# Kernel optimization log

Measured on AMD Instinct MI355X. Metric: run time of the kernel, lower is better.

The kernel has to match this reference:

```python
import jax, jax.numpy as jnp
import numpy as np

N = 100000      # nodes
EG = 600000     # global (knn) edges used by GAT layers
E = 600000      # prediction edges scored by edge_mlp
H = 1           # gat_heads
C = 64          # hidden_dim (per-head out channels)
HC = H * C
EDGE_IN = 2 * HC + 2  # 130
EDGE_HID = EDGE_IN * 4  # 520


def gat_layer(x, W, att_src, att_dst, bias, src, dst):
    # PyG GATConv (concat=True, residual=False, no edge_dim, eval mode)
    n = x.shape[0]
    h = (x @ W).reshape(n, H, C)                      # [N,H,C]
    a_s = jnp.sum(h * att_src, axis=-1)               # [N,H]
    a_d = jnp.sum(h * att_dst, axis=-1)               # [N,H]
    alpha = jax.nn.leaky_relu(a_s[src] + a_d[dst], 0.2)  # [Eg,H]
    amax = jax.ops.segment_max(alpha, dst, num_segments=n)
    amax = jnp.where(jnp.isfinite(amax), amax, 0.0)
    e = jnp.exp(alpha - amax[dst])
    denom = jax.ops.segment_sum(e, dst, num_segments=n)
    w = e / (denom[dst] + 1e-16)                      # scatter-softmax over in-edges of dst
    out = jax.ops.segment_sum(h[src] * w[:, :, None], dst, num_segments=n)
    return out.reshape(n, HC) + bias


def setup_inputs() -> dict:
    key = jax.random.key(0)
    ks = jax.random.split(key, 16)
    glorot = lambda k, shape: jax.random.normal(k, shape, jnp.float32) * np.sqrt(2.0 / (shape[0] + shape[-1]))
    inp = {
        "pos": jax.random.normal(ks[0], (N, 3), jnp.float32),
        "edge_index": jax.random.randint(ks[1], (2, E), 0, N, jnp.int32),
        "global_edge_index": jax.random.randint(ks[2], (2, EG), 0, N, jnp.int32),
        "edge_attr": jax.random.uniform(ks[3], (E, 2), jnp.float32),
        # GAT layer 0 (in=3)
        "W0": glorot(ks[4], (3, HC)),
        "att_src0": glorot(ks[5], (1, H, C)),
        "att_dst0": glorot(ks[6], (1, H, C)),
        "b0": jnp.zeros((HC,), jnp.float32),
        # GAT layer 1 (in=HC)
        "W1": glorot(ks[7], (HC, HC)),
        "att_src1": glorot(ks[8], (1, H, C)),
        "att_dst1": glorot(ks[9], (1, H, C)),
        "b1": jnp.zeros((HC,), jnp.float32),
        # edge MLP: Linear(130,520) -> ELU -> Linear(520,1)
        "Wm1": glorot(ks[10], (EDGE_IN, EDGE_HID)),
        "bm1": jnp.zeros((EDGE_HID,), jnp.float32),
        "Wm2": glorot(ks[11], (EDGE_HID, 1)),
        "bm2": jnp.zeros((1,), jnp.float32),
    }
    return inp


def reference(pos, edge_index, global_edge_index, edge_attr,
              W0, att_src0, att_dst0, b0,
              W1, att_src1, att_dst1, b1,
              Wm1, bm1, Wm2, bm2):
    gsrc, gdst = global_edge_index[0], global_edge_index[1]
    x = pos  # dropout p=0 -> identity
    x = jax.nn.elu(gat_layer(x, W0, att_src0, att_dst0, b0, gsrc, gdst))
    x = jax.nn.elu(gat_layer(x, W1, att_src1, att_dst1, b1, gsrc, gdst))
    # per-edge gather-concat-MLP
    esrc, edst = edge_index[0], edge_index[1]
    ef = jnp.concatenate([x[esrc], x[edst], edge_attr], axis=1)  # [E, 130]
    h = jax.nn.elu(ef @ Wm1 + bm1)
    edge_values = (h @ Wm2 + bm2)[:, 0]  # [E]
    return edge_values
```

## Files before the change

### kernel.cpp

```cpp
#include <hip/hip_runtime.h>

#define KN 100000
#define KEG 600000
#define KE 600000
#define NB 98
#define LOG2E 1.4426950408889634f
#define LN2 0.6931471805599453f

#define FB_PREP 391
#define FB_CVEC 33
#define FB_HIST 2344
#define FB_T0 25000

using u16 = unsigned short;
typedef __bf16 bf16x8 __attribute__((ext_vector_type(8)));
typedef float f32x4 __attribute__((ext_vector_type(4)));
typedef float f32x2 __attribute__((ext_vector_type(2)));

__device__ __forceinline__ float b2f(u16 u) { return __uint_as_float(((unsigned)u) << 16); }
__device__ __forceinline__ u16 f2b(float f) {
  unsigned u = __float_as_uint(f);
  u += 0x7FFF + ((u >> 16) & 1);
  return (u16)(u >> 16);
}
__device__ __forceinline__ int imin(int a, int b) { return a < b ? a : b; }
__device__ __forceinline__ float fexp2(float x) {
#if __has_builtin(__builtin_amdgcn_exp2f)
  return __builtin_amdgcn_exp2f(x);
#else
  return __expf(x * LN2);
#endif
}

__device__ __forceinline__ void gload_lds16(const void* g, void* l) {
  __builtin_amdgcn_global_load_lds(
      (const __attribute__((address_space(1))) unsigned int*)g,
      (__attribute__((address_space(3))) unsigned int*)l,
      16, 0, 0);
}

__global__ __launch_bounds__(256) void k_front(
    const float* __restrict__ pos, const float* __restrict__ W0,
    const float* __restrict__ att_s, const float* __restrict__ att_d,
    const float* __restrict__ wm1, const float* __restrict__ bm1,
    const float* __restrict__ wm2, const float* __restrict__ w1,
    const int* __restrict__ gdst,
    u16* __restrict__ wm1t, u16* __restrict__ w1t, float2* __restrict__ wsc2,
    float* __restrict__ w2sum, int* __restrict__ counts,
    u16* __restrict__ h, float* __restrict__ a_s, float* __restrict__ a_d) {
  int bid = blockIdx.x;
  if (bid < FB_PREP) {
    int idx = bid * 256 + threadIdx.x;
    if (idx < 33 * 5 * 512) {
      int j = idx & 7;
      int lane = (idx >> 3) & 63;
      int f = (idx >> 9) % 5;
      int nt = idx / (512 * 5);
      int n = nt * 16 + (lane & 15);
      float v = 0.f;
      if (n < 520) {
        if (f < 4) {
          int k = f * 32 + (lane >> 4) * 8 + j;
          v = wm1[k * 520 + n] * LOG2E;
        } else {
          int kk = (lane >> 4) * 8 + j;
          if (kk == 0) v = wm1[128 * 520 + n] * LOG2E;
          else if (kk == 1) v = wm1[129 * 520 + n] * LOG2E;
          else if (kk == 2) v = bm1[n] * LOG2E;
        }
      }
      wm1t[idx] = f2b(v);
    }
    if (idx < 33 * 64) {
      int lane = idx & 63, nt = idx >> 6;
      int col = nt * 16 + (lane & 15);
      float w2 = (col < 520) ? wm2[col] : 0.f;
      float2 p; p.x = w2; p.y = -LN2 * w2;
      wsc2[idx] = p;
    }
    if (idx < 4 * 2 * 64 * 8) {
      int j = idx & 7;
      int lane = (idx >> 3) & 63;
      int kt = (idx >> 9) & 1;
      int nt = idx >> 10;
      int n = nt * 16 + (lane & 15);
      int k = kt * 32 + (lane >> 4) * 8 + j;
      w1t[idx] = f2b(w1[k * 64 + n]);
    }
  } else if (bid < FB_PREP + FB_CVEC) {
    int lane = threadIdx.x & 63;
    int w = (bid - FB_PREP) * 4 + (threadIdx.x >> 6);
    float x = 0.f;
    if (w <= 129) {
      const float* row = wm1 + (size_t)w * 520;
#pragma unroll
      for (int j = 0; j < 8; ++j) x += row[j * 64 + lane] * wm2[j * 64 + lane];
      if (lane < 8) x += row[512 + lane] * wm2[512 + lane];
    } else if (w == 130) {
#pragma unroll
      for (int j = 0; j < 8; ++j) x += bm1[j * 64 + lane] * wm2[j * 64 + lane];
      if (lane < 8) x += bm1[512 + lane] * wm2[512 + lane];
    } else if (w == 131) {
#pragma unroll
      for (int j = 0; j < 8; ++j) x += wm2[j * 64 + lane];
      if (lane < 8) x += wm2[512 + lane];
    }
    for (int off = 1; off < 64; off <<= 1) x += __shfl_xor(x, off);
    if (w <= 130 && lane < 16) {
      int f = w >> 5, kk = w & 31;
      int qq = kk >> 3, jj = kk & 7;
      u16 chi = f2b(x);
      float v = (lane == 0) ? x : (lane == 1 ? (x - b2f(chi)) : 0.f);
      wm1t[(33 * 5 + f) * 512 + (qq * 16 + lane) * 8 + jj] = f2b(v);
    } else if (w == 131 && lane == 0) {
      w2sum[0] = x;
    }
  } else if (bid < FB_PREP + FB_CVEC + FB_HIST) {
    int e = (bid - (FB_PREP + FB_CVEC)) * 256 + threadIdx.x;
    if (e < KEG) atomicAdd(counts + gdst[e], 1);
  } else {
    int lane = threadIdx.x & 63;
    int n = (bid - (FB_PREP + FB_CVEC + FB_HIST)) * 4 + (threadIdx.x >> 6);
    float p0 = pos[n * 3 + 0], p1 = pos[n * 3 + 1], p2 = pos[n * 3 + 2];
    float hv = p0 * W0[lane] + p1 * W0[64 + lane] + p2 * W0[128 + lane];
    h[n * 64 + lane] = f2b(hv);
    float s = hv * att_s[lane];
    float d = hv * att_d[lane];
    for (int off = 1; off < 64; off <<= 1) { s += __shfl_xor(s, off); d += __shfl_xor(d, off); }
    if (lane == 0) { a_s[n] = s; a_d[n] = d; }
  }
}


__global__ __launch_bounds__(1024) void k_scan_block(
    const int* __restrict__ counts, int* __restrict__ incl, int* __restrict__ bsum) {
  int gid = blockIdx.x * 1024 + threadIdx.x;
  int lane = threadIdx.x & 63, w = threadIdx.x >> 6;
  int x = (gid < KN) ? counts[gid] : 0;
  for (int off = 1; off < 64; off <<= 1) {
    int y = __shfl_up(x, off);
    if (lane >= off) x += y;
  }
  __shared__ int wtot[16];
  if (lane == 63) wtot[w] = x;
  __syncthreads();
  if (w == 0 && lane < 16) {
    int t = wtot[lane];
    for (int off = 1; off < 16; off <<= 1) {
      int y = __shfl_up(t, off);
      if (lane >= off) t += y;
    }
    wtot[lane] = t;
  }
  __syncthreads();
  if (w > 0) x += wtot[w - 1];
  if (gid < KN) incl[gid] = x;
  if (threadIdx.x == 1023) bsum[blockIdx.x] = x;
}

__global__ __launch_bounds__(64) void k_scan_bsum(const int* __restrict__ bsum, int* __restrict__ boff) {
  int lane = threadIdx.x;
  int x0 = (lane < NB) ? bsum[lane] : 0;
  int x1 = (64 + lane < NB) ? bsum[64 + lane] : 0;
  int i0 = x0, i1 = x1;
  for (int off = 1; off < 64; off <<= 1) {
    int y0 = __shfl_up(i0, off), y1 = __shfl_up(i1, off);
    if (lane >= off) { i0 += y0; i1 += y1; }
  }
  int tot0 = __shfl(i0, 63);
  if (lane < NB) boff[lane] = i0 - x0;
  if (64 + lane < NB) boff[64 + lane] = i1 - x1 + tot0;
}

__global__ __launch_bounds__(1024) void k_scan_final(
    const int* __restrict__ incl, const int* __restrict__ counts,
    const int* __restrict__ boff, int* __restrict__ row_start) {
  int gid = blockIdx.x * 1024 + threadIdx.x;
  if (gid < KN) row_start[gid] = incl[gid] - counts[gid] + boff[blockIdx.x];
}

__global__ __launch_bounds__(256) void k_fill(
    const int* __restrict__ gsrc, const int* __restrict__ gdst,
    const int* __restrict__ row_start, int* __restrict__ cursor,
    int* __restrict__ csr_src) {
  int e = blockIdx.x * 256 + threadIdx.x;
  if (e >= KEG) return;
  int d = gdst[e];
  int pos = atomicAdd(cursor + d, 1);
  csr_src[row_start[d] + pos] = gsrc[e];
}


__global__ __launch_bounds__(256) void k_aggt1(
    const int* __restrict__ row_start, const int* __restrict__ counts,
    const int* __restrict__ csr_src, const float* __restrict__ a_s0,
    const float* __restrict__ a_d0, const u16* __restrict__ h0,
    const float* __restrict__ b0, const u16* __restrict__ w1t,
    const float* __restrict__ as1, const float* __restrict__ ad1,
    u16* __restrict__ h1, float* __restrict__ a_s1, float* __restrict__ a_d1) {
  __shared__ u16 xb[64][72];
  int lane = threadIdx.x & 63;
  int wave = threadIdx.x >> 6;
  int nb = blockIdx.x * 64;
  int nodebase = nb + wave * 16;

  for (int i = 0; i < 16; ++i) {
    int n = nodebase + i;
    float v = 0.f;
    if (n < KN) {
      int start = row_start[n], deg = counts[n];
      float adn = a_d0[n];
      float acc = 0.f, den = 0.f;
      int j = 0;
      for (; j + 4 <= deg; j += 4) {
        int s0 = csr_src[start + j];
        int s1 = csr_src[start + j + 1];
        int s2 = csr_src[start + j + 2];
        int s3 = csr_src[start + j + 3];
        float al0 = a_s0[s0] + adn; al0 = al0 > 0.f ? al0 : 0.2f * al0;
        float al1 = a_s0[s1] + adn; al1 = al1 > 0.f ? al1 : 0.2f * al1;
        float al2 = a_s0[s2] + adn; al2 = al2 > 0.f ? al2 : 0.2f * al2;
        float al3 = a_s0[s3] + adn; al3 = al3 > 0.f ? al3 : 0.2f * al3;
        float w0 = __expf(al0), w1 = __expf(al1);
        float w2 = __expf(al2), w3 = __expf(al3);
        float h0v = b2f(h0[s0 * 64 + lane]);
        float h1v = b2f(h0[s1 * 64 + lane]);
        float h2v = b2f(h0[s2 * 64 + lane]);
        float h3v = b2f(h0[s3 * 64 + lane]);
        den += (w0 + w1) + (w2 + w3);
        acc += w0 * h0v + w1 * h1v + w2 * h2v + w3 * h3v;
      }
      for (; j < deg; ++j) {
        int s0 = csr_src[start + j];
        float al = a_s0[s0] + adn; al = al > 0.f ? al : 0.2f * al;
        float w0 = __expf(al);
        den += w0;
        acc += w0 * b2f(h0[s0 * 64 + lane]);
      }
      v = acc / (den + 1e-16f) + b0[lane];
      v = v > 0.f ? v : expm1f(v);
    }
    xb[wave * 16 + i][lane] = f2b(v);
  }

  int m = lane & 15, q = lane >> 4;
  const u16* row = xb[wave * 16 + m];
  bf16x8 A0 = *(const bf16x8*)(row + q * 8);
  bf16x8 A1 = *(const bf16x8*)(row + 32 + q * 8);

  const bf16x8* bt = (const bf16x8*)w1t;
  float ps[4] = {0.f, 0.f, 0.f, 0.f};
  float pd[4] = {0.f, 0.f, 0.f, 0.f};
#pragma unroll
  for (int nt = 0; nt < 4; ++nt) {
    int col = nt * 16 + m;
    float asv = as1[col], adv = ad1[col];
    f32x4 acc = {0.f, 0.f, 0.f, 0.f};
    acc = __builtin_amdgcn_mfma_f32_16x16x32_bf16(A0, bt[(nt * 2 + 0) * 64 + lane], acc, 0, 0, 0);
    acc = __builtin_amdgcn_mfma_f32_16x16x32_bf16(A1, bt[(nt * 2 + 1) * 64 + lane], acc, 0, 0, 0);
#pragma unroll
    for (int r = 0; r < 4; ++r) {
      int rown = nodebase + q * 4 + r;
      if (rown < KN) h1[rown * 64 + col] = f2b(acc[r]);
      ps[r] += acc[r] * asv;
      pd[r] += acc[r] * adv;
    }
  }
#pragma unroll
  for (int r = 0; r < 4; ++r) {
    float s = ps[r], d = pd[r];
    s += __shfl_xor(s, 1); d += __shfl_xor(d, 1);
    s += __shfl_xor(s, 2); d += __shfl_xor(d, 2);
    s += __shfl_xor(s, 4); d += __shfl_xor(d, 4);
    s += __shfl_xor(s, 8); d += __shfl_xor(d, 8);
    int rown = nodebase + q * 4 + r;
    if (m == 0 && rown < KN) { a_s1[rown] = s; a_d1[rown] = d; }
  }
}

__global__ __launch_bounds__(256) void k_gat_agg(
    const int* __restrict__ row_start, const int* __restrict__ counts,
    const int* __restrict__ csr_src, const float* __restrict__ a_s,
    const float* __restrict__ a_d, const u16* __restrict__ h,
    const float* __restrict__ bias, u16* __restrict__ xout) {
  int lane = threadIdx.x & 63;
  int n = blockIdx.x * 4 + (threadIdx.x >> 6);
  int start = row_start[n], deg = counts[n];
  float adn = a_d[n];
  float acc = 0.f, den = 0.f;
  int j = 0;
  for (; j + 4 <= deg; j += 4) {
    int s0 = csr_src[start + j];
    int s1 = csr_src[start + j + 1];
    int s2 = csr_src[start + j + 2];
    int s3 = csr_src[start + j + 3];
    float al0 = a_s[s0] + adn; al0 = al0 > 0.f ? al0 : 0.2f * al0;
    float al1 = a_s[s1] + adn; al1 = al1 > 0.f ? al1 : 0.2f * al1;
    float al2 = a_s[s2] + adn; al2 = al2 > 0.f ? al2 : 0.2f * al2;
    float al3 = a_s[s3] + adn; al3 = al3 > 0.f ? al3 : 0.2f * al3;
    float w0 = __expf(al0), w1 = __expf(al1);
    float w2 = __expf(al2), w3 = __expf(al3);
    float h0 = b2f(h[s0 * 64 + lane]);
    float h1 = b2f(h[s1 * 64 + lane]);
    float h2 = b2f(h[s2 * 64 + lane]);
    float h3 = b2f(h[s3 * 64 + lane]);
    den += (w0 + w1) + (w2 + w3);
    acc += w0 * h0 + w1 * h1 + w2 * h2 + w3 * h3;
  }
  for (; j < deg; ++j) {
    int s0 = csr_src[start + j];
    float al = a_s[s0] + adn; al = al > 0.f ? al : 0.2f * al;
    float w0 = __expf(al);
    den += w0;
    acc += w0 * b2f(h[s0 * 64 + lane]);
  }
  float v = acc / (den + 1e-16f) + bias[lane];
  v = v > 0.f ? v : expm1f(v);
  xout[n * 64 + lane] = f2b(v);
}

__global__ __launch_bounds__(256) void k_edge_mlp(
    const int* __restrict__ eidx, const u16* __restrict__ x2bf,
    const float* __restrict__ eattr, const u16* __restrict__ wm1t,
    const float2* __restrict__ wsc2, const float* __restrict__ w2sum,
    const float* __restrict__ bm2, float* __restrict__ out) {
  __shared__ uint4 Bbuf[2][20 * 64];
  int tid = threadIdx.x;
  int lane = tid & 63;
  int wave = tid >> 6;
  int base = blockIdx.x * 256 + wave * 64;
  int m = lane & 15, q = lane >> 4;

  const uint4* gB = (const uint4*)wm1t;
#pragma unroll
  for (int k = 0; k < 5; ++k)
    gload_lds16(gB + tid + k * 256, &Bbuf[0][tid + k * 256]);

  bf16x8 A[4][4];
#pragma unroll
  for (int s = 0; s < 4; ++s) {
    int row = imin(base + s * 16 + m, KE - 1);
    int es = eidx[row], ed = eidx[KE + row];
    const bf16x8* psrc = (const bf16x8*)(x2bf + es * 64);
    const bf16x8* pdst = (const bf16x8*)(x2bf + ed * 64);
    A[s][0] = psrc[q];
    A[s][1] = psrc[q + 4];
    A[s][2] = pdst[q];
    A[s][3] = pdst[q + 4];
  }
  bf16x8 A5[4];
#pragma unroll
  for (int s = 0; s < 4; ++s) {
    bf16x8 a5 = {0, 0, 0, 0, 0, 0, 0, 0};
    if (q == 0) {
      int row = imin(base + s * 16 + m, KE - 1);
      a5[0] = (__bf16)eattr[row * 2 + 0];
      a5[1] = (__bf16)eattr[row * 2 + 1];
      a5[2] = (__bf16)1.0f;
    }
    A5[s] = a5;
  }

  f32x2 osum[4][2];
#pragma unroll
  for (int s = 0; s < 4; ++s) {
    osum[s][0] = (f32x2){0.f, 0.f};
    osum[s][1] = (f32x2){0.f, 0.f};
  }

  __syncthreads();

#pragma unroll 1
  for (int ch = 0; ch < 9; ++ch) {
    int cur = ch & 1, nxt = cur ^ 1;
    if (ch < 8) {
      const uint4* gs = gB + (ch + 1) * 1280;
#pragma unroll
      for (int k = 0; k < 5; ++k)
        gload_lds16(gs + tid + k * 256, &Bbuf[nxt][tid + k * 256]);
    }
    int lim = (ch == 8) ? 1 : 4;
#pragma unroll 1
    for (int li = 0; li < lim; ++li) {
      int nt = ch * 4 + li;
      const bf16x8* lb = (const bf16x8*)(Bbuf[cur] + li * 5 * 64);
      bf16x8 B0 = lb[0 * 64 + lane];
      bf16x8 B1 = lb[1 * 64 + lane];
      bf16x8 B2 = lb[2 * 64 + lane];
      bf16x8 B3 = lb[3 * 64 + lane];
      bf16x8 B4 = lb[4 * 64 + lane];
      float2 w2 = wsc2[nt * 64 + lane];
#pragma unroll
      for (int s = 0; s < 4; ++s) {
        f32x4 acc = {0.f, 0.f, 0.f, 0.f};
        acc = __builtin_amdgcn_mfma_f32_16x16x32_bf16(A[s][0], B0, acc, 0, 0, 0);
        acc = __builtin_amdgcn_mfma_f32_16x16x32_bf16(A[s][1], B1, acc, 0, 0, 0);
        acc = __builtin_amdgcn_mfma_f32_16x16x32_bf16(A[s][2], B2, acc, 0, 0, 0);
        acc = __builtin_amdgcn_mfma_f32_16x16x32_bf16(A[s][3], B3, acc, 0, 0, 0);
        acc = __builtin_amdgcn_mfma_f32_16x16x32_bf16(A5[s],   B4, acc, 0, 0, 0);
        f32x2 t0 = {fminf(acc[0], 0.f), fminf(acc[1], 0.f)};
        f32x2 t1 = {fminf(acc[2], 0.f), fminf(acc[3], 0.f)};
        f32x2 e0 = {fexp2(t0.x), fexp2(t0.y)};
        f32x2 e1 = {fexp2(t1.x), fexp2(t1.y)};
        osum[s][0] += e0 * w2.x + t0 * w2.y;
        osum[s][1] += e1 * w2.x + t1 * w2.y;
      }
    }
    if (ch < 8) __syncthreads();
  }

  const bf16x8* bt = (const bf16x8*)wm1t;
  bf16x8 L0 = bt[(33 * 5 + 0) * 64 + lane];
  bf16x8 L1 = bt[(33 * 5 + 1) * 64 + lane];
  bf16x8 L2 = bt[(33 * 5 + 2) * 64 + lane];
  bf16x8 L3 = bt[(33 * 5 + 3) * 64 + lane];
  bf16x8 L4 = bt[(33 * 5 + 4) * 64 + lane];
  float w2s = w2sum[0];
  float b2v = bm2[0];

#pragma unroll
  for (int s = 0; s < 4; ++s) {
    f32x4 accL = {0.f, 0.f, 0.f, 0.f};
    accL = __builtin_amdgcn_mfma_f32_16x16x32_bf16(A[s][0], L0, accL, 0, 0, 0);
    accL = __builtin_amdgcn_mfma_f32_16x16x32_bf16(A[s][1], L1, accL, 0, 0, 0);
    accL = __builtin_amdgcn_mfma_f32_16x16x32_bf16(A[s][2], L2, accL, 0, 0, 0);
    accL = __builtin_amdgcn_mfma_f32_16x16x32_bf16(A[s][3], L3, accL, 0, 0, 0);
    accL = __builtin_amdgcn_mfma_f32_16x16x32_bf16(A5[s],   L4, accL, 0, 0, 0);
    float ov[4] = {osum[s][0].x, osum[s][0].y, osum[s][1].x, osum[s][1].y};
#pragma unroll
    for (int r = 0; r < 4; ++r) {
      float lin = accL[r] + __shfl_xor(accL[r], 1);
      float v = ov[r];
      v += __shfl_xor(v, 1);
      v += __shfl_xor(v, 2);
      v += __shfl_xor(v, 4);
      v += __shfl_xor(v, 8);
      if (m == 0) {
        int row = base + s * 16 + q * 4 + r;
        if (row < KE) out[row] = v - w2s + lin + b2v;
      }
    }
  }
}

extern "C" void kernel_launch(void* const* d_in, const int* in_sizes, int n_in,
                              void* d_out, int out_size, void* d_ws, size_t ws_size,
                              hipStream_t stream) {
  const float* pos  = (const float*)d_in[0];
  const int* eidx   = (const int*)d_in[1];
  const int* geidx  = (const int*)d_in[2];
  const float* eattr= (const float*)d_in[3];
  const float* W0   = (const float*)d_in[4];
  const float* as0  = (const float*)d_in[5];
  const float* ad0  = (const float*)d_in[6];
  const float* b0   = (const float*)d_in[7];
  const float* W1   = (const float*)d_in[8];
  const float* as1  = (const float*)d_in[9];
  const float* ad1  = (const float*)d_in[10];
  const float* b1   = (const float*)d_in[11];
  const float* Wm1  = (const float*)d_in[12];
  const float* bm1  = (const float*)d_in[13];
  const float* Wm2  = (const float*)d_in[14];
  const float* bm2  = (const float*)d_in[15];
  float* out = (float*)d_out;

  char* ws = (char*)d_ws;
  size_t off = 0;
  auto carve = [&](size_t bytes) {
    char* p = ws + off;
    off = (off + bytes + 255) & ~(size_t)255;
    return p;
  };
  int* counts    = (int*)carve((size_t)KN * 4);
  int* cursor    = (int*)carve((size_t)KN * 4);
  int* incl      = (int*)carve((size_t)KN * 4);
  int* row_start = (int*)carve((size_t)KN * 4);
  int* bsum      = (int*)carve(128 * 4);
  int* boff      = (int*)carve(128 * 4);
  int* csr_src   = (int*)carve((size_t)KEG * 4);
  u16* h0        = (u16*)carve((size_t)KN * 64 * 2);
  u16* h1        = (u16*)carve((size_t)KN * 64 * 2);
  u16* x12       = (u16*)carve((size_t)KN * 64 * 2);
  float* a_s0    = (float*)carve((size_t)KN * 4);
  float* a_d0    = (float*)carve((size_t)KN * 4);
  float* a_s1    = (float*)carve((size_t)KN * 4);
  float* a_d1    = (float*)carve((size_t)KN * 4);
  u16* wm1t      = (u16*)carve((size_t)36 * 5 * 512 * 2);
  u16* w1t       = (u16*)carve((size_t)4 * 2 * 64 * 8 * 2);
  float2* wsc2   = (float2*)carve((size_t)33 * 64 * 8);
  float* w2sum   = (float*)carve(256);

  const int* gsrc = geidx;
  const int* gdst = geidx + KEG;

  hipMemsetAsync(d_ws, 0, 800128, stream);

  k_front<<<FB_PREP + FB_CVEC + FB_HIST + FB_T0, 256, 0, stream>>>(
      pos, W0, as0, ad0, Wm1, bm1, Wm2, W1, gdst,
      wm1t, w1t, wsc2, w2sum, counts, h0, a_s0, a_d0);

  k_scan_block<<<NB, 1024, 0, stream>>>(counts, incl, bsum);
  k_scan_bsum<<<1, 64, 0, stream>>>(bsum, boff);
  k_scan_final<<<NB, 1024, 0, stream>>>(incl, counts, boff, row_start);
  k_fill<<<(KEG + 255) / 256, 256, 0, stream>>>(gsrc, gdst, row_start, cursor, csr_src);

  k_aggt1<<<(KN + 63) / 64, 256, 0, stream>>>(row_start, counts, csr_src,
                                              a_s0, a_d0, h0, b0,
                                              w1t, as1, ad1, h1, a_s1, a_d1);

  k_gat_agg<<<KN / 4, 256, 0, stream>>>(row_start, counts, csr_src, a_s1, a_d1, h1, b1, x12);

  k_edge_mlp<<<(KE + 255) / 256, 256, 0, stream>>>(eidx, x12, eattr, wm1t, wsc2, w2sum, bm2, out);
}
```

Baseline: 386.0 us.

## Fuse block-offset scan into final scan and halve edge MLP weight chunks

The single-wave k_scan_bsum launch is removed. Every k_scan_final block now recomputes the block-sum prefix in shared memory, which saves one launch and one dependency at the cost of redundant per-block work. The edge MLP weight staging moves from 4-tile to 2-tile chunks, halving the LDS double buffer to raise occupancy, in exchange for twice as many loop iterations and barriers. The final linear-term tile is now read from LDS, after the last prefetch, instead of from global memory, and the wm1t allocation shrinks to match.

Result: slower. 398.0 us (+3.1%).

```diff
diff --git a/kernel.cpp b/kernel.cpp
--- a/kernel.cpp
+++ b/kernel.cpp
@@ -158,25 +158,26 @@
   if (threadIdx.x == 1023) bsum[blockIdx.x] = x;
 }
 
-__global__ __launch_bounds__(64) void k_scan_bsum(const int* __restrict__ bsum, int* __restrict__ boff) {
-  int lane = threadIdx.x;
-  int x0 = (lane < NB) ? bsum[lane] : 0;
-  int x1 = (64 + lane < NB) ? bsum[64 + lane] : 0;
-  int i0 = x0, i1 = x1;
-  for (int off = 1; off < 64; off <<= 1) {
-    int y0 = __shfl_up(i0, off), y1 = __shfl_up(i1, off);
-    if (lane >= off) { i0 += y0; i1 += y1; }
-  }
-  int tot0 = __shfl(i0, 63);
-  if (lane < NB) boff[lane] = i0 - x0;
-  if (64 + lane < NB) boff[64 + lane] = i1 - x1 + tot0;
-}
-
 __global__ __launch_bounds__(1024) void k_scan_final(
     const int* __restrict__ incl, const int* __restrict__ counts,
-    const int* __restrict__ boff, int* __restrict__ row_start) {
+    const int* __restrict__ bsum, int* __restrict__ row_start) {
+  __shared__ int sboff[128];
+  if (threadIdx.x < 64) {
+    int lane = threadIdx.x;
+    int x0 = (lane < NB) ? bsum[lane] : 0;
+    int x1 = (64 + lane < NB) ? bsum[64 + lane] : 0;
+    int i0 = x0, i1 = x1;
+    for (int off = 1; off < 64; off <<= 1) {
+      int y0 = __shfl_up(i0, off), y1 = __shfl_up(i1, off);
+      if (lane >= off) { i0 += y0; i1 += y1; }
+    }
+    int tot0 = __shfl(i0, 63);
+    sboff[lane] = i0 - x0;
+    sboff[64 + lane] = i1 - x1 + tot0;
+  }
+  __syncthreads();
   int gid = blockIdx.x * 1024 + threadIdx.x;
-  if (gid < KN) row_start[gid] = incl[gid] - counts[gid] + boff[blockIdx.x];
+  if (gid < KN) row_start[gid] = incl[gid] - counts[gid] + sboff[blockIdx.x];
 }
 
 __global__ __launch_bounds__(256) void k_fill(
@@ -324,7 +325,7 @@
     const float* __restrict__ eattr, const u16* __restrict__ wm1t,
     const float2* __restrict__ wsc2, const float* __restrict__ w2sum,
     const float* __restrict__ bm2, float* __restrict__ out) {
-  __shared__ uint4 Bbuf[2][20 * 64];
+  __shared__ uint4 Bbuf[2][640];
   int tid = threadIdx.x;
   int lane = tid & 63;
   int wave = tid >> 6;
@@ -332,9 +333,12 @@
   int m = lane & 15, q = lane >> 4;
 
   const uint4* gB = (const uint4*)wm1t;
-#pragma unroll
-  for (int k = 0; k < 5; ++k)
-    gload_lds16(gB + tid + k * 256, &Bbuf[0][tid + k * 256]);
+  {
+    int s0 = wave * 160 + lane;
+    gload_lds16(gB + s0, &Bbuf[0][s0]);
+    gload_lds16(gB + s0 + 64, &Bbuf[0][s0 + 64]);
+    if (lane < 32) gload_lds16(gB + s0 + 128, &Bbuf[0][s0 + 128]);
+  }
 
   bf16x8 A[4][4];
 #pragma unroll
@@ -371,19 +375,20 @@
   __syncthreads();
 
 #pragma unroll 1
-  for (int ch = 0; ch < 9; ++ch) {
+  for (int ch = 0; ch < 17; ++ch) {
     int cur = ch & 1, nxt = cur ^ 1;
-    if (ch < 8) {
-      const uint4* gs = gB + (ch + 1) * 1280;
-#pragma unroll
-      for (int k = 0; k < 5; ++k)
-        gload_lds16(gs + tid + k * 256, &Bbuf[nxt][tid + k * 256]);
-    }
-    int lim = (ch == 8) ? 1 : 4;
+    if (ch < 16) {
+      const uint4* gs = gB + (ch + 1) * 640;
+      int s0 = wave * 160 + lane;
+      gload_lds16(gs + s0, &Bbuf[nxt][s0]);
+      gload_lds16(gs + s0 + 64, &Bbuf[nxt][s0 + 64]);
+      if (lane < 32) gload_lds16(gs + s0 + 128, &Bbuf[nxt][s0 + 128]);
+    }
+    int lim = (ch == 16) ? 1 : 2;
 #pragma unroll 1
     for (int li = 0; li < lim; ++li) {
-      int nt = ch * 4 + li;
-      const bf16x8* lb = (const bf16x8*)(Bbuf[cur] + li * 5 * 64);
+      int nt = ch * 2 + li;
+      const bf16x8* lb = (const bf16x8*)(&Bbuf[cur][li * 320]);
       bf16x8 B0 = lb[0 * 64 + lane];
       bf16x8 B1 = lb[1 * 64 + lane];
       bf16x8 B2 = lb[2 * 64 + lane];
@@ -406,15 +411,15 @@
         osum[s][1] += e1 * w2.x + t1 * w2.y;
       }
     }
-    if (ch < 8) __syncthreads();
-  }
-
-  const bf16x8* bt = (const bf16x8*)wm1t;
-  bf16x8 L0 = bt[(33 * 5 + 0) * 64 + lane];
-  bf16x8 L1 = bt[(33 * 5 + 1) * 64 + lane];
-  bf16x8 L2 = bt[(33 * 5 + 2) * 64 + lane];
-  bf16x8 L3 = bt[(33 * 5 + 3) * 64 + lane];
-  bf16x8 L4 = bt[(33 * 5 + 4) * 64 + lane];
+    if (ch < 16) __syncthreads();
+  }
+
+  const bf16x8* lbL = (const bf16x8*)(&Bbuf[0][320]);
+  bf16x8 L0 = lbL[0 * 64 + lane];
+  bf16x8 L1 = lbL[1 * 64 + lane];
+  bf16x8 L2 = lbL[2 * 64 + lane];
+  bf16x8 L3 = lbL[3 * 64 + lane];
+  bf16x8 L4 = lbL[4 * 64 + lane];
   float w2s = w2sum[0];
   float b2v = bm2[0];
 
@@ -476,7 +481,6 @@
   int* incl      = (int*)carve((size_t)KN * 4);
   int* row_start = (int*)carve((size_t)KN * 4);
   int* bsum      = (int*)carve(128 * 4);
-  int* boff      = (int*)carve(128 * 4);
   int* csr_src   = (int*)carve((size_t)KEG * 4);
   u16* h0        = (u16*)carve((size_t)KN * 64 * 2);
   u16* h1        = (u16*)carve((size_t)KN * 64 * 2);
@@ -485,7 +489,7 @@
   float* a_d0    = (float*)carve((size_t)KN * 4);
   float* a_s1    = (float*)carve((size_t)KN * 4);
   float* a_d1    = (float*)carve((size_t)KN * 4);
-  u16* wm1t      = (u16*)carve((size_t)36 * 5 * 512 * 2);
+  u16* wm1t      = (u16*)carve((size_t)34 * 5 * 512 * 2);
   u16* w1t       = (u16*)carve((size_t)4 * 2 * 64 * 8 * 2);
   float2* wsc2   = (float2*)carve((size_t)33 * 64 * 8);
   float* w2sum   = (float*)carve(256);
@@ -500,8 +504,7 @@
       wm1t, w1t, wsc2, w2sum, counts, h0, a_s0, a_d0);
 
   k_scan_block<<<NB, 1024, 0, stream>>>(counts, incl, bsum);
-  k_scan_bsum<<<1, 64, 0, stream>>>(bsum, boff);
-  k_scan_final<<<NB, 1024, 0, stream>>>(incl, counts, boff, row_start);
+  k_scan_final<<<NB, 1024, 0, stream>>>(incl, counts, bsum, row_start);
   k_fill<<<(KEG + 255) / 256, 256, 0, stream>>>(gsrc, gdst, row_start, cursor, csr_src);
 
   k_aggt1<<<(KN + 63) / 64, 256, 0, stream>>>(row_start, counts, csr_src,
```
